# Kernel optimization log

Measured on AMD Instinct MI355X. Metric: run time of the kernel, lower is better.

The kernel has to match this reference:

```python
import jax, jax.numpy as jnp
import numpy as np

B, S, DIM, H = 2, 2048, 1024, 16
DH = DIM // H


def setup_inputs() -> dict:
    key = jax.random.key(0)
    ks = jax.random.split(key, 12)
    sd = 0.02
    inp = {
        "query": jax.random.normal(ks[0], (B, S, DIM), jnp.float32),
        "key": jax.random.normal(ks[1], (B, S, DIM), jnp.float32),
        "value": jax.random.normal(ks[2], (B, S, DIM), jnp.float32),
        "pad_mask": jax.random.randint(ks[3], (B, 1, 1, S), 0, 2, jnp.int32),
        "training_status": 1,
        "Wq": jax.random.normal(ks[4], (DIM, DIM), jnp.float32) * sd,
        "bq": jnp.zeros((DIM,), jnp.float32),
        "Wk": jax.random.normal(ks[5], (DIM, DIM), jnp.float32) * sd,
        "bk": jnp.zeros((DIM,), jnp.float32),
        "Wv": jax.random.normal(ks[6], (DIM, DIM), jnp.float32) * sd,
        "bv": jnp.zeros((DIM,), jnp.float32),
        "Wf": jax.random.normal(ks[7], (DIM, DIM), jnp.float32) * sd,
        "bf": jnp.zeros((DIM,), jnp.float32),
    }
    return inp


def reference(query, key, value, pad_mask, training_status, Wq, bq, Wk, bk, Wv, bv, Wf, bf):
    b, s, _ = query.shape
    # projections, split heads -> [B, H, S, Dh]
    def split_heads(x):
        return x.reshape(b, -1, H, DH).transpose(0, 2, 1, 3)

    q = split_heads(query @ Wq + bq)
    k = split_heads(key @ Wk + bk)
    v = split_heads(value @ Wv + bv)

    # NOTE: original divides by sqrt(Dh) twice (explicit + self.scale) => /Dh
    scores = jnp.einsum("bhqd,bhkd->bhqk", q, k) / jnp.asarray(DH, q.dtype)
    if training_status:
        scores = jnp.where(pad_mask == 0, jnp.asarray(-1e9, scores.dtype), scores)
    attn = jax.nn.softmax(scores, axis=-1)
    out = jnp.einsum("bhqk,bhkd->bhqd", attn, v)  # [B,H,S,Dh]
    out = out.transpose(0, 2, 1, 3).reshape(b, s, DIM)
    return out @ Wf + bf
```

## Files before the change

### kernel.cpp

```cpp
#include <hip/hip_runtime.h>

#define Bn   2
#define Sn   2048
#define DIMn 1024
#define Hn   16
#define DHn  64

typedef unsigned short u16;
typedef unsigned int   u32;

typedef __attribute__((ext_vector_type(8))) __bf16 bf16x8;
typedef __attribute__((ext_vector_type(8))) float  f32x8v;
typedef __attribute__((ext_vector_type(4))) float  f32x4;

__device__ __forceinline__ u16 f2bf(float f) {
    union { __bf16 h; u16 u; } v; v.h = (__bf16)f; return v.u;
}
__device__ __forceinline__ bf16x8 ldfrag(const u16* p) {
    union { uint4 u; bf16x8 v; } x;
    x.u = *(const uint4*)p;
    return x.v;
}
__device__ __forceinline__ uint4 pack8(const u16 h[8]) {
    uint4 r;
    r.x = (u32)h[0] | ((u32)h[1] << 16);
    r.y = (u32)h[2] | ((u32)h[3] << 16);
    r.z = (u32)h[4] | ((u32)h[5] << 16);
    r.w = (u32)h[6] | ((u32)h[7] << 16);
    return r;
}
__device__ __forceinline__ void gl_lds16(const void* g, void* l) {
    __builtin_amdgcn_global_load_lds(
        (const __attribute__((address_space(1))) void*)g,
        (__attribute__((address_space(3))) void*)l, 16, 0, 0);
}
__device__ __forceinline__ void barrier_nodrain() {
    asm volatile("" ::: "memory");
    __builtin_amdgcn_s_barrier();
    asm volatile("" ::: "memory");
}

__global__ __launch_bounds__(256) void prep_weights(
    const float* __restrict__ Wq, const float* __restrict__ Wk,
    const float* __restrict__ Wv, const float* __restrict__ Wf,
    u16* __restrict__ Wt)
{
    __shared__ __align__(16) float tile[64][68];
    const float* W = (blockIdx.z == 0) ? Wq : (blockIdx.z == 1) ? Wk
                   : (blockIdx.z == 2) ? Wv : Wf;
    const int t = threadIdx.x;
    const int n0 = blockIdx.x * 64, k0 = blockIdx.y * 64;
    const int rr = t >> 4, cc = (t & 15) * 4;
#pragma unroll
    for (int i = 0; i < 4; i++)
        *(float4*)&tile[rr + 16 * i][cc] =
            *(const float4*)(W + (size_t)(k0 + rr + 16 * i) * DIMn + n0 + cc);
    __syncthreads();
#pragma unroll
    for (int e = 0; e < 2; e++) {
        const int ci = 2 * t + e;
        const int nn = ci >> 3, kc = ci & 7;
        const int n = n0 + nn, k = k0 + kc * 8;
        u16 h[8];
#pragma unroll
        for (int j = 0; j < 8; j++) h[j] = f2bf(tile[kc * 8 + j][nn]);
        const int X = n >> 7, o = (n >> 4) & 7, l15 = n & 15;
        const int T = k >> 5, quad = (k >> 3) & 3;
        const size_t off =
            ((((size_t)(blockIdx.z * 8 + X) * 32 + T) * 8 + o) * 64 + quad * 16 + l15) * 8;
        *(uint4*)(Wt + off) = pack8(h);
    }
}

__global__ __launch_bounds__(256) void gemm_qkv(
    const float* __restrict__ Aq, const float* __restrict__ Ak,
    const float* __restrict__ Av, const u16* __restrict__ Wt,
    const float* __restrict__ bqp, const float* __restrict__ bkp,
    const float* __restrict__ bvp, u16* __restrict__ Qw,
    u16* __restrict__ Kw, u16* __restrict__ VwT)
{
    __shared__ union {
        struct { __align__(16) u16 Abf[2][4096];
                 __align__(16) u16 Bbf[2][4096]; } s;
        __align__(16) u16 Ep[32][144];
    } L;

    const int f = blockIdx.x;
    const int xcd = f & 7;
    const int q = f >> 3;
    const int z = q >> 5;
    const int rem = q & 31;
    const int yi = rem >> 3, x = rem & 7;
    const int y = xcd * 4 + yi;
    const int m0 = y * 128, n0 = x * 128;

    const float* A    = (z == 0) ? Aq  : (z == 1) ? Ak  : Av;
    const float* bias = (z == 0) ? bqp : (z == 1) ? bkp : bvp;

    const int t = threadIdx.x;
    const int lane = t & 63, wave = t >> 6;
    const int quad = lane >> 4, l15 = lane & 15;
    const int wm = wave >> 1, wn = wave & 1;

    const float* baseA[2];
#pragma unroll
    for (int s = 0; s < 2; s++)
        baseA[s] = A + (size_t)(m0 + (wave * 2 + s) * 16 + l15) * DIMn + quad * 8;
    const u16* baseB[2];
#pragma unroll
    for (int s = 0; s < 2; s++)
        baseB[s] = Wt + ((size_t)((z * 8 + x) * 32) * 8 + (wave * 2 + s)) * 512 + lane * 8;

    auto LOADA = [&](int tt, uint4 (&ar)[4]) {
#pragma unroll
        for (int s = 0; s < 2; s++) {
            const float* p = baseA[s] + tt * 32;
            ar[2 * s]     = *(const uint4*)(p);
            ar[2 * s + 1] = *(const uint4*)(p + 4);
        }
    };
    auto STAGEB = [&](int tt, int buf) {
#pragma unroll
        for (int s = 0; s < 2; s++)
            gl_lds16(baseB[s] + (size_t)tt * 4096, &L.s.Bbf[buf][(wave * 2 + s) * 512]);
    };
    auto CVTWRITE = [&](uint4 (&ar)[4], int buf) {
#pragma unroll
        for (int s = 0; s < 2; s++) {
            union { uint4 u[2]; f32x8v f; } cv;
            cv.u[0] = ar[2 * s]; cv.u[1] = ar[2 * s + 1];
            union { bf16x8 v; uint4 u; } hv;
            hv.v = __builtin_convertvector(cv.f, bf16x8);
            *(uint4*)&L.s.Abf[buf][(wave * 2 + s) * 512 + lane * 8] = hv.u;
        }
    };

    f32x4 acc[4][4];
#pragma unroll
    for (int i = 0; i < 4; i++)
#pragma unroll
        for (int j = 0; j < 4; j++) acc[i][j] = (f32x4){0.f, 0.f, 0.f, 0.f};

    const int NT = DIMn / 32;
    uint4 ra[4], rb[4];
    LOADA(0, ra); STAGEB(0, 0);
    LOADA(1, rb); STAGEB(1, 1);

    auto ITER = [&](int tt, uint4 (&ar)[4], int buf) {
        if (tt < NT - 1) asm volatile("s_waitcnt vmcnt(6)" ::: "memory");
        else             asm volatile("s_waitcnt vmcnt(0)" ::: "memory");
        CVTWRITE(ar, buf);
        asm volatile("s_waitcnt lgkmcnt(0)" ::: "memory");
        barrier_nodrain();

        bf16x8 a[4], b[4];
#pragma unroll
        for (int i = 0; i < 4; i++)
            a[i] = ldfrag(&L.s.Abf[buf][((wm * 4 + i) * 4 + quad) * 128 + l15 * 8]);
#pragma unroll
        for (int j = 0; j < 4; j++)
            b[j] = ldfrag(&L.s.Bbf[buf][((wn * 4 + j) * 4 + quad) * 128 + l15 * 8]);
#pragma unroll
        for (int i = 0; i < 4; i++)
#pragma unroll
            for (int j = 0; j < 4; j++)
                acc[i][j] = __builtin_amdgcn_mfma_f32_16x16x32_bf16(a[i], b[j], acc[i][j], 0, 0, 0);

        asm volatile("s_waitcnt lgkmcnt(0)" ::: "memory");
        barrier_nodrain();
        if (tt + 2 < NT) { LOADA(tt + 2, ar); STAGEB(tt + 2, buf); }
    };
    for (int tt = 0; tt < NT; tt += 2) { ITER(tt, ra, 0); ITER(tt + 1, rb, 1); }

    float bv[4];
#pragma unroll
    for (int j = 0; j < 4; j++) bv[j] = bias[n0 + wn * 64 + j * 16 + l15];

    const int bb = y >> 4;

    if (z == 0) {
#pragma unroll
        for (int i = 0; i < 4; i++) {
            __syncthreads();
#pragma unroll
            for (int j = 0; j < 4; j++)
#pragma unroll
                for (int r = 0; r < 4; r++)
                    L.Ep[wm * 16 + quad * 4 + r][wn * 64 + j * 16 + l15] =
                        f2bf(acc[i][j][r] + bv[j]);
            __syncthreads();
#pragma unroll
            for (int e = 0; e < 2; e++) {
                const int ci = t + 256 * e;
                const int row = ci >> 4, c = ci & 15;
                const uint4 v = *(const uint4*)&L.Ep[row][c * 8];
                const int m = m0 + (row >> 4) * 64 + i * 16 + (row & 15);
                const int ss = m & 2047;
                const int n = n0 + c * 8;
                const int hh = n >> 6, dd = n & 63;
                *(uint4*)(Qw + ((size_t)(bb * Hn + hh) * Sn + ss) * DHn + dd) = v;
            }
        }
    } else if (z == 1) {
#pragma unroll
        for (int i = 0; i < 4; i++) {
            __syncthreads();
#pragma unroll
            for (int j = 0; j < 4; j++)
#pragma unroll
                for (int r = 0; r < 4; r++)
                    L.Ep[wm * 16 + quad * 4 + r][wn * 64 + j * 16 + l15] =
                        f2bf(acc[i][j][r] + bv[j]);
            __syncthreads();
#pragma unroll
            for (int e2 = 0; e2 < 2; e2++) {
                const int tid = t + 256 * e2;
                const int l15o = tid & 15;
                const int qo   = (tid >> 4) & 3;
                const int k1   = (tid >> 6) & 1;
                const int c3   = (tid >> 7) & 1;
                const int w    = (tid >> 8) & 1;
                const int c    = c3 * 8 + k1 * 4 + qo;
                const uint4 v = *(const uint4*)&L.Ep[w * 16 + l15o][c * 8];
                const int ss = (m0 & 2047) + w * 64 + i * 16 + l15o;
                const int hh = (n0 + c * 8) >> 6;
                const int jt = ss >> 6;
                const int o  = i * 2 + k1;
                const size_t off =
                    ((((size_t)(bb * Hn + hh) * 32 + jt) * 8 + o) * 64 + qo * 16 + l15o) * 8;
                *(uint4*)(Kw + off) = v;
            }
        }
    } else {
#pragma unroll
        for (int j = 0; j < 4; j++) {
            __syncthreads();
#pragma unroll
            for (int i = 0; i < 4; i++) {
                u16 h4[4];
#pragma unroll
                for (int r = 0; r < 4; r++) h4[r] = f2bf(acc[i][j][r] + bv[j]);
                uint2 pk;
                pk.x = (u32)h4[0] | ((u32)h4[1] << 16);
                pk.y = (u32)h4[2] | ((u32)h4[3] << 16);
                *(uint2*)&L.Ep[wn * 16 + l15][wm * 64 + i * 16 + quad * 4] = pk;
            }
            __syncthreads();
#pragma unroll
            for (int e2 = 0; e2 < 2; e2++) {
                const int tid = t + 256 * e2;
                const int l15o = tid & 15;
                const int qo   = (tid >> 4) & 3;
                const int k1   = (tid >> 6) & 1;
                const int c3   = (tid >> 7) & 1;
                const int w    = (tid >> 8) & 1;
                const int c    = c3 * 8 + k1 * 4 + qo;
                const uint4 v = *(const uint4*)&L.Ep[w * 16 + l15o][c * 8];
                const int n  = n0 + w * 64 + j * 16 + l15o;
                const int hh = n >> 6;
                const int jt = ((m0 & 2047) >> 6) + c3;
                const int o  = j * 2 + k1;
                const size_t off =
                    ((((size_t)(bb * Hn + hh) * 32 + jt) * 8 + o) * 64 + qo * 16 + l15o) * 8;
                *(uint4*)(VwT + off) = v;
            }
        }
    }
}

__global__ __launch_bounds__(256) void gemm_final(
    const u16* __restrict__ A, const u16* __restrict__ Bt,
    const float* __restrict__ bias, float* __restrict__ out)
{
    __shared__ __align__(16) u16 Abf[3][32 * 128];
    __shared__ __align__(16) u16 Bbf[3][32 * 128];

    const int f = blockIdx.x;
    const int xcd = f & 7, q = f >> 3;
    const int y = xcd * 4 + (q >> 3), x = q & 7;
    const int m0 = y * 128, n0 = x * 128;

    const int t = threadIdx.x;
    const int lane = t & 63, wave = t >> 6;
    const int quad = lane >> 4, l15 = lane & 15;
    const int wm = wave >> 1, wn = wave & 1;

    int arow[2], aq[2];
#pragma unroll
    for (int s = 0; s < 2; s++) {
        const int c = wave * 8 + s * 4 + quad;
        arow[s] = (c >> 2) * 16 + l15;
        aq[s] = c & 3;
    }
    const u16* baseB[2];
#pragma unroll
    for (int s = 0; s < 2; s++)
        baseB[s] = Bt + ((size_t)(x * 32) * 8 + (wave * 2 + s)) * 512 + lane * 8;

    auto STAGE = [&](int tt, int buf) {
        const int hh = tt >> 1, d64 = (tt & 1) * 32;
#pragma unroll
        for (int s = 0; s < 2; s++) {
            const int m = m0 + arow[s], bb = m >> 11, ss = m & 2047;
            const u16* gp = A + ((size_t)(bb * Hn + hh) * Sn + ss) * DHn + d64 + aq[s] * 8;
            gl_lds16(gp, &Abf[buf][(wave * 8 + s * 4) * 128]);
        }
#pragma unroll
        for (int s = 0; s < 2; s++)
            gl_lds16(baseB[s] + (size_t)tt * 4096, &Bbf[buf][(wave * 8 + s * 4) * 128]);
    };

    f32x4 acc[4][4];
#pragma unroll
    for (int i = 0; i < 4; i++)
#pragma unroll
        for (int j = 0; j < 4; j++) acc[i][j] = (f32x4){0.f, 0.f, 0.f, 0.f};

    const int NT = DIMn / 32;
    STAGE(0, 0);
    STAGE(1, 1);
    STAGE(2, 2);

    int buf = 0;
    for (int tt = 0; tt < NT; ++tt) {
        if (tt < NT - 2)       asm volatile("s_waitcnt vmcnt(8)" ::: "memory");
        else if (tt == NT - 2) asm volatile("s_waitcnt vmcnt(4)" ::: "memory");
        else                   asm volatile("s_waitcnt vmcnt(0)" ::: "memory");
        barrier_nodrain();

        bf16x8 a[4], b[4];
#pragma unroll
        for (int i = 0; i < 4; i++)
            a[i] = ldfrag(&Abf[buf][((wm * 4 + i) * 4 + quad) * 128 + l15 * 8]);
#pragma unroll
        for (int j = 0; j < 4; j++)
            b[j] = ldfrag(&Bbf[buf][((wn * 4 + j) * 4 + quad) * 128 + l15 * 8]);
#pragma unroll
        for (int i = 0; i < 4; i++)
#pragma unroll
            for (int j = 0; j < 4; j++)
                acc[i][j] = __builtin_amdgcn_mfma_f32_16x16x32_bf16(a[i], b[j], acc[i][j], 0, 0, 0);

        asm volatile("s_waitcnt lgkmcnt(0)" ::: "memory");
        barrier_nodrain();
        if (tt + 3 < NT) STAGE(tt + 3, buf);
        buf = (buf == 2) ? 0 : buf + 1;
    }

    float bv[4];
#pragma unroll
    for (int j = 0; j < 4; j++) bv[j] = bias[n0 + wn * 64 + j * 16 + l15];

#pragma unroll
    for (int i = 0; i < 4; i++)
#pragma unroll
        for (int j = 0; j < 4; j++) {
            const int n = n0 + wn * 64 + j * 16 + l15;
#pragma unroll
            for (int r = 0; r < 4; r++) {
                const int m = m0 + wm * 64 + i * 16 + quad * 4 + r;
                out[(size_t)m * DIMn + n] = acc[i][j][r] + bv[j];
            }
        }
}

__global__ __launch_bounds__(256) void attn_mfma(
    const u16* __restrict__ Qw, const u16* __restrict__ Kw,
    const u16* __restrict__ VwT, const int* __restrict__ mask,
    const int* __restrict__ tstat, u16* __restrict__ Aw)
{
    __shared__ __align__(16) u16 Kbf[2][32 * 128];
    __shared__ __align__(16) u16 Vbf[2][32 * 128];
    __shared__ __align__(16) u16 Ps[64 * 64];

    const int f = blockIdx.x;
    const int xcd = f & 7, q = f >> 3;
    const int p = xcd * 4 + (q >> 5);
    const int qt = q & 31;
    const int b = p >> 4, h = p & 15;
    const int q0 = qt * 64;

    const int t = threadIdx.x;
    const int lane = t & 63, wave = t >> 6;
    const int quad = lane >> 4, l15 = lane & 15;
    const bool use_mask = (tstat[0] != 0);
    const size_t slab = (size_t)(b * Hn + h) * Sn * DHn;

    const size_t hbase = (size_t)(b * Hn + h) * 32 * 8 * 512;
    const u16* baseK[2];
    const u16* baseV[2];
#pragma unroll
    for (int s = 0; s < 2; s++) {
        const int o = wave * 2 + s;
        baseK[s] = Kw  + hbase + (size_t)o * 512 + lane * 8;
        baseV[s] = VwT + hbase + (size_t)o * 512 + lane * 8;
    }

    {
        const int4* msrc4 = (const int4*)(mask + (size_t)b * Sn);
        int4* mdst4 = (int4*)&Kbf[0][0];
        mdst4[t]       = msrc4[t];
        mdst4[t + 256] = msrc4[t + 256];
    }
    bf16x8 aq[2];
#pragma unroll
    for (int ks = 0; ks < 2; ks++) {
        union { uint4 u; bf16x8 v; } xx;
        xx.u = *(const uint4*)(Qw + slab + (size_t)(q0 + wave * 16 + l15) * DHn + ks * 32 + quad * 8);
        aq[ks] = xx.v;
    }
    __syncthreads();

    u32 mw0 = 0, mw1 = 0, mw2 = 0, mw3 = 0;
    {
        const int* ml = (const int*)&Kbf[0][0];
#pragma unroll
        for (int k = 0; k < 128; k++) {
            const u32 bit = (ml[k * 16 + l15] != 0) ? 1u : 0u;
            if (k < 32)      mw0 |= bit << k;
            else if (k < 64) mw1 |= bit << (k - 32);
            else if (k < 96) mw2 |= bit << (k - 64);
            else             mw3 |= bit << (k - 96);
        }
    }
    __syncthreads();

    auto STAGE = [&](int tt, int buf) {
#pragma unroll
        for (int s = 0; s < 2; s++) {
            gl_lds16(baseK[s] + (size_t)tt * 4096, &Kbf[buf][(wave * 8 + s * 4) * 128]);
            gl_lds16(baseV[s] + (size_t)tt * 4096, &Vbf[buf][(wave * 8 + s * 4) * 128]);
        }
    };

    float lsum[4] = {0.f, 0.f, 0.f, 0.f};
    f32x4 O[4];
#pragma unroll
    for (int dt = 0; dt < 4; dt++) O[dt] = (f32x4){0.f, 0.f, 0.f, 0.f};

    const int NT = Sn / 64;
    STAGE(0, 0);
    STAGE(1, 1);

#pragma unroll 2
    for (int tt = 0; tt < NT; ++tt) {
        const int buf = tt & 1;
        if (tt < NT - 1) asm volatile("s_waitcnt vmcnt(4)" ::: "memory");
        else             asm volatile("s_waitcnt vmcnt(0)" ::: "memory");
        barrier_nodrain();

        f32x4 s[4];
#pragma unroll
        for (int ct = 0; ct < 4; ct++) s[ct] = (f32x4){0.f, 0.f, 0.f, 0.f};
        __builtin_amdgcn_s_setprio(1);
#pragma unroll
        for (int ct = 0; ct < 4; ct++)
#pragma unroll
            for (int ks = 0; ks < 2; ks++) {
                const bf16x8 bk = ldfrag(&Kbf[buf][(ct * 8 + ks * 4 + quad) * 128 + l15 * 8]);
                s[ct] = __builtin_amdgcn_mfma_f32_16x16x32_bf16(aq[ks], bk, s[ct], 0, 0, 0);
            }
        __builtin_amdgcn_s_setprio(0);

        const int wsel = tt >> 3;
        const u32 cw = (wsel == 0) ? mw0 : (wsel == 1) ? mw1 : (wsel == 2) ? mw2 : mw3;
        const int sh = (tt & 7) * 4;
        u32 mc[4];
#pragma unroll
        for (int ct = 0; ct < 4; ct++)
            mc[ct] = use_mask ? ((cw >> (sh + ct)) & 1u) : 1u;

#pragma unroll
        for (int ct = 0; ct < 4; ct++)
#pragma unroll
            for (int r = 0; r < 4; r++) {
                const float sv = mc[ct] ? s[ct][r] * (1.0f / 64.0f) : -1e9f;
                const float pp = __expf(sv);
                lsum[r] += pp;
                const int prow = wave * 16 + quad * 4 + r;
                Ps[prow * 64 + ((ct * 16 + l15) ^ ((prow & 7) << 3))] = f2bf(pp);
            }
        asm volatile("s_waitcnt lgkmcnt(0)" ::: "memory");

        bf16x8 pa[2];
        const int rrow = wave * 16 + l15;
#pragma unroll
        for (int kc = 0; kc < 2; kc++)
            pa[kc] = ldfrag(&Ps[rrow * 64 + ((kc * 32 + quad * 8) ^ ((l15 & 7) << 3))]);
        __builtin_amdgcn_s_setprio(1);
#pragma unroll
        for (int dt = 0; dt < 4; dt++)
#pragma unroll
            for (int kc = 0; kc < 2; kc++) {
                const bf16x8 bvv = ldfrag(&Vbf[buf][(dt * 8 + kc * 4 + quad) * 128 + l15 * 8]);
                O[dt] = __builtin_amdgcn_mfma_f32_16x16x32_bf16(pa[kc], bvv, O[dt], 0, 0, 0);
            }
        __builtin_amdgcn_s_setprio(0);

        asm volatile("s_waitcnt lgkmcnt(0)" ::: "memory");
        barrier_nodrain();
        if (tt + 2 < NT) STAGE(tt + 2, buf);
    }

#pragma unroll
    for (int r = 0; r < 4; r++) {
#pragma unroll
        for (int off = 1; off < 16; off <<= 1) lsum[r] += __shfl_xor(lsum[r], off);
    }
    float linv[4];
#pragma unroll
    for (int r = 0; r < 4; r++) linv[r] = 1.0f / fmaxf(lsum[r], 1e-30f);

    __syncthreads();
#pragma unroll
    for (int r = 0; r < 4; r++)
#pragma unroll
        for (int dt = 0; dt < 4; dt++)
            Ps[(wave * 16 + quad * 4 + r) * 64 + dt * 16 + l15] = f2bf(O[dt][r] * linv[r]);
    __syncthreads();
#pragma unroll
    for (int e2 = 0; e2 < 2; e2++) {
        const int tid = t + 256 * e2;
        const int lr = tid >> 3, c16 = tid & 7;
        const uint4 v = *(const uint4*)&Ps[lr * 64 + c16 * 8];
        *(uint4*)(Aw + slab + (size_t)(q0 + lr) * DHn + c16 * 8) = v;
    }
}

extern "C" void kernel_launch(void* const* d_in, const int* in_sizes, int n_in,
                              void* d_out, int out_size, void* d_ws, size_t ws_size,
                              hipStream_t stream) {
    const float* query = (const float*)d_in[0];
    const float* key   = (const float*)d_in[1];
    const float* value = (const float*)d_in[2];
    const int*   pmask = (const int*)d_in[3];
    const int*   tstat = (const int*)d_in[4];
    const float* Wq  = (const float*)d_in[5];
    const float* bq  = (const float*)d_in[6];
    const float* Wk  = (const float*)d_in[7];
    const float* bk  = (const float*)d_in[8];
    const float* Wv  = (const float*)d_in[9];
    const float* bv  = (const float*)d_in[10];
    const float* Wf  = (const float*)d_in[11];
    const float* bfb = (const float*)d_in[12];
    float* outp = (float*)d_out;

    const size_t NT = (size_t)Bn * Sn * DIMn;
    u16* Qw  = (u16*)d_ws;
    u16* Kw  = Qw + NT;
    u16* VwT = Kw + NT;
    u16* Wt  = VwT + NT;
    const size_t WSZ = (size_t)DIMn * DIMn;

    prep_weights<<<dim3(16, 16, 4), 256, 0, stream>>>(Wq, Wk, Wv, Wf, Wt);

    gemm_qkv<<<768, 256, 0, stream>>>(query, key, value, Wt, bq, bk, bv, Qw, Kw, VwT);

    attn_mfma<<<1024, 256, 0, stream>>>(Qw, Kw, VwT, pmask, tstat, Qw);

    gemm_final<<<256, 256, 0, stream>>>(Qw, Wt + 3 * WSZ, bfb, outp);
}
```

Before: 278.0 us.

## Store attention output in MFMA-fragment layout and retile final GEMM to 128x64

The attention kernel now writes its normalized output in a pre-swizzled fragment-major layout. The final projection GEMM can then fetch contiguous 512-element chunks directly, with no per-row address math. The final GEMM moves to 128x64 tiles with K=64 per stage, double buffering and 512 blocks, which aims at better occupancy and fewer, larger loads. Separately, the attention kernel drops its s_setprio hints and folds the mask into an additive bias feeding a single fmaf before exp.

```diff
diff --git a/kernel.cpp b/kernel.cpp
--- a/kernel.cpp
+++ b/kernel.cpp
@@ -272,90 +272,103 @@
     const u16* __restrict__ A, const u16* __restrict__ Bt,
     const float* __restrict__ bias, float* __restrict__ out)
 {
-    __shared__ __align__(16) u16 Abf[3][32 * 128];
-    __shared__ __align__(16) u16 Bbf[3][32 * 128];
+    __shared__ __align__(16) u16 Abf[2][16 * 512];
+    __shared__ __align__(16) u16 Bbf[2][8 * 512];
 
     const int f = blockIdx.x;
     const int xcd = f & 7, q = f >> 3;
-    const int y = xcd * 4 + (q >> 3), x = q & 7;
-    const int m0 = y * 128, n0 = x * 128;
+    const int y = xcd * 4 + (q >> 4);
+    const int x = q & 15;
+    const int m0 = y * 128, n0 = x * 64;
+    const int bb = y >> 4;
+    const int jtb = (y & 15) * 2;
 
     const int t = threadIdx.x;
     const int lane = t & 63, wave = t >> 6;
     const int quad = lane >> 4, l15 = lane & 15;
     const int wm = wave >> 1, wn = wave & 1;
 
-    int arow[2], aq[2];
+    const u16* baseA[4];
+#pragma unroll
+    for (int s = 0; s < 4; s++) {
+        const int c = wave * 4 + s;
+        const int g = c >> 1, dsub = c & 1;
+        const int jt2 = g >> 2, sub16 = g & 3;
+        baseA[s] = A + (((size_t)(bb * Hn) * 32 + jtb + jt2) * 8 + (sub16 * 2 + dsub)) * 512
+                     + lane * 8;
+    }
+    const u16* baseB[2];
 #pragma unroll
     for (int s = 0; s < 2; s++) {
-        const int c = wave * 8 + s * 4 + quad;
-        arow[s] = (c >> 2) * 16 + l15;
-        aq[s] = c & 3;
-    }
-    const u16* baseB[2];
-#pragma unroll
-    for (int s = 0; s < 2; s++)
-        baseB[s] = Bt + ((size_t)(x * 32) * 8 + (wave * 2 + s)) * 512 + lane * 8;
+        const int cb = wave * 2 + s;
+        const int os = cb >> 1, ksub = cb & 1;
+        baseB[s] = Bt + (((size_t)(x >> 1) * 32 + ksub) * 8 + ((x & 1) * 4 + os)) * 512
+                      + lane * 8;
+    }
 
     auto STAGE = [&](int tt, int buf) {
-        const int hh = tt >> 1, d64 = (tt & 1) * 32;
-#pragma unroll
-        for (int s = 0; s < 2; s++) {
-            const int m = m0 + arow[s], bb = m >> 11, ss = m & 2047;
-            const u16* gp = A + ((size_t)(bb * Hn + hh) * Sn + ss) * DHn + d64 + aq[s] * 8;
-            gl_lds16(gp, &Abf[buf][(wave * 8 + s * 4) * 128]);
-        }
+#pragma unroll
+        for (int s = 0; s < 4; s++)
+            gl_lds16(baseA[s] + (size_t)tt * 131072, &Abf[buf][(wave * 4 + s) * 512]);
 #pragma unroll
         for (int s = 0; s < 2; s++)
-            gl_lds16(baseB[s] + (size_t)tt * 4096, &Bbf[buf][(wave * 8 + s * 4) * 128]);
+            gl_lds16(baseB[s] + (size_t)tt * 8192, &Bbf[buf][(wave * 2 + s) * 512]);
     };
 
-    f32x4 acc[4][4];
+    f32x4 acc[4][2];
 #pragma unroll
     for (int i = 0; i < 4; i++)
 #pragma unroll
-        for (int j = 0; j < 4; j++) acc[i][j] = (f32x4){0.f, 0.f, 0.f, 0.f};
-
-    const int NT = DIMn / 32;
+        for (int j = 0; j < 2; j++) acc[i][j] = (f32x4){0.f, 0.f, 0.f, 0.f};
+
+    const int NT = 16;
     STAGE(0, 0);
     STAGE(1, 1);
-    STAGE(2, 2);
-
-    int buf = 0;
+
     for (int tt = 0; tt < NT; ++tt) {
-        if (tt < NT - 2)       asm volatile("s_waitcnt vmcnt(8)" ::: "memory");
-        else if (tt == NT - 2) asm volatile("s_waitcnt vmcnt(4)" ::: "memory");
-        else                   asm volatile("s_waitcnt vmcnt(0)" ::: "memory");
+        const int buf = tt & 1;
+        if (tt < NT - 1) asm volatile("s_waitcnt vmcnt(6)" ::: "memory");
+        else             asm volatile("s_waitcnt vmcnt(0)" ::: "memory");
         barrier_nodrain();
 
-        bf16x8 a[4], b[4];
+        bf16x8 a[4][2], b[2][2];
 #pragma unroll
         for (int i = 0; i < 4; i++)
-            a[i] = ldfrag(&Abf[buf][((wm * 4 + i) * 4 + quad) * 128 + l15 * 8]);
-#pragma unroll
-        for (int j = 0; j < 4; j++)
-            b[j] = ldfrag(&Bbf[buf][((wn * 4 + j) * 4 + quad) * 128 + l15 * 8]);
+#pragma unroll
+            for (int ks = 0; ks < 2; ks++) {
+                const int c = (wm * 4 + i) * 2 + ks;
+                a[i][ks] = ldfrag(&Abf[buf][c * 512 + (quad * 16 + l15) * 8]);
+            }
+#pragma unroll
+        for (int j = 0; j < 2; j++)
+#pragma unroll
+            for (int ks = 0; ks < 2; ks++) {
+                const int cb = (wn * 2 + j) * 2 + ks;
+                b[j][ks] = ldfrag(&Bbf[buf][cb * 512 + (quad * 16 + l15) * 8]);
+            }
 #pragma unroll
         for (int i = 0; i < 4; i++)
 #pragma unroll
-            for (int j = 0; j < 4; j++)
-                acc[i][j] = __builtin_amdgcn_mfma_f32_16x16x32_bf16(a[i], b[j], acc[i][j], 0, 0, 0);
+            for (int j = 0; j < 2; j++)
+#pragma unroll
+                for (int ks = 0; ks < 2; ks++)
+                    acc[i][j] = __builtin_amdgcn_mfma_f32_16x16x32_bf16(
+                        a[i][ks], b[j][ks], acc[i][j], 0, 0, 0);
 
         asm volatile("s_waitcnt lgkmcnt(0)" ::: "memory");
         barrier_nodrain();
-        if (tt + 3 < NT) STAGE(tt + 3, buf);
-        buf = (buf == 2) ? 0 : buf + 1;
-    }
-
-    float bv[4];
-#pragma unroll
-    for (int j = 0; j < 4; j++) bv[j] = bias[n0 + wn * 64 + j * 16 + l15];
+        if (tt + 2 < NT) STAGE(tt + 2, buf);
+    }
+
+    float bv[2];
+#pragma unroll
+    for (int j = 0; j < 2; j++) bv[j] = bias[n0 + wn * 32 + j * 16 + l15];
 
 #pragma unroll
     for (int i = 0; i < 4; i++)
 #pragma unroll
-        for (int j = 0; j < 4; j++) {
-            const int n = n0 + wn * 64 + j * 16 + l15;
+        for (int j = 0; j < 2; j++) {
+            const int n = n0 + wn * 32 + j * 16 + l15;
 #pragma unroll
             for (int r = 0; r < 4; r++) {
                 const int m = m0 + wm * 64 + i * 16 + quad * 4 + r;
@@ -452,7 +465,6 @@
         f32x4 s[4];
 #pragma unroll
         for (int ct = 0; ct < 4; ct++) s[ct] = (f32x4){0.f, 0.f, 0.f, 0.f};
-        __builtin_amdgcn_s_setprio(1);
 #pragma unroll
         for (int ct = 0; ct < 4; ct++)
 #pragma unroll
@@ -460,22 +472,20 @@
                 const bf16x8 bk = ldfrag(&Kbf[buf][(ct * 8 + ks * 4 + quad) * 128 + l15 * 8]);
                 s[ct] = __builtin_amdgcn_mfma_f32_16x16x32_bf16(aq[ks], bk, s[ct], 0, 0, 0);
             }
-        __builtin_amdgcn_s_setprio(0);
 
         const int wsel = tt >> 3;
         const u32 cw = (wsel == 0) ? mw0 : (wsel == 1) ? mw1 : (wsel == 2) ? mw2 : mw3;
         const int sh = (tt & 7) * 4;
-        u32 mc[4];
+        float badd[4];
 #pragma unroll
         for (int ct = 0; ct < 4; ct++)
-            mc[ct] = use_mask ? ((cw >> (sh + ct)) & 1u) : 1u;
+            badd[ct] = (!use_mask || ((cw >> (sh + ct)) & 1u)) ? 0.0f : -1e9f;
 
 #pragma unroll
         for (int ct = 0; ct < 4; ct++)
 #pragma unroll
             for (int r = 0; r < 4; r++) {
-                const float sv = mc[ct] ? s[ct][r] * (1.0f / 64.0f) : -1e9f;
-                const float pp = __expf(sv);
+                const float pp = __expf(fmaf(s[ct][r], 1.0f / 64.0f, badd[ct]));
                 lsum[r] += pp;
                 const int prow = wave * 16 + quad * 4 + r;
                 Ps[prow * 64 + ((ct * 16 + l15) ^ ((prow & 7) << 3))] = f2bf(pp);
@@ -487,7 +497,6 @@
 #pragma unroll
         for (int kc = 0; kc < 2; kc++)
             pa[kc] = ldfrag(&Ps[rrow * 64 + ((kc * 32 + quad * 8) ^ ((l15 & 7) << 3))]);
-        __builtin_amdgcn_s_setprio(1);
 #pragma unroll
         for (int dt = 0; dt < 4; dt++)
 #pragma unroll
@@ -495,7 +504,6 @@
                 const bf16x8 bvv = ldfrag(&Vbf[buf][(dt * 8 + kc * 4 + quad) * 128 + l15 * 8]);
                 O[dt] = __builtin_amdgcn_mfma_f32_16x16x32_bf16(pa[kc], bvv, O[dt], 0, 0, 0);
             }
-        __builtin_amdgcn_s_setprio(0);
 
         asm volatile("s_waitcnt lgkmcnt(0)" ::: "memory");
         barrier_nodrain();
@@ -518,12 +526,15 @@
         for (int dt = 0; dt < 4; dt++)
             Ps[(wave * 16 + quad * 4 + r) * 64 + dt * 16 + l15] = f2bf(O[dt][r] * linv[r]);
     __syncthreads();
+    const size_t cbase = ((size_t)(b * Hn + h) * 32 + qt) * 4096;
 #pragma unroll
     for (int e2 = 0; e2 < 2; e2++) {
         const int tid = t + 256 * e2;
-        const int lr = tid >> 3, c16 = tid & 7;
-        const uint4 v = *(const uint4*)&Ps[lr * 64 + c16 * 8];
-        *(uint4*)(Aw + slab + (size_t)(q0 + lr) * DHn + c16 * 8) = v;
+        const int row = tid >> 3, cg = tid & 7;
+        const int sub16 = row >> 4, dsub = cg >> 2, quadk = cg & 3;
+        const uint4 v = *(const uint4*)&Ps[row * 64 + cg * 8];
+        *(uint4*)(Aw + cbase + (size_t)(sub16 * 2 + dsub) * 512
+                  + (quadk * 16 + (row & 15)) * 8) = v;
     }
 }
 
@@ -558,5 +569,5 @@
 
     attn_mfma<<<1024, 256, 0, stream>>>(Qw, Kw, VwT, pmask, tstat, Qw);
 
-    gemm_final<<<256, 256, 0, stream>>>(Qw, Wt + 3 * WSZ, bfb, outp);
-}
+    gemm_final<<<512, 256, 0, stream>>>(Qw, Wt + 3 * WSZ, bfb, outp);
+}
```

Result: faster. 271.2 us (-2.4%).
